# Optimization experiments

Hardware: AMD Instinct MI355X
Metric: run time of the kernel (lower is better)

Reference implementation:

```python
import jax, jax.numpy as jnp
import numpy as np

N = 40000          # nodes
E = 640000         # edges
D_IN, D_HID, D_EMB, D_OUT = 128, 128, 64, 2


def glorot(key, shape):
    lim = np.sqrt(6.0 / (shape[0] + shape[1]))
    return jax.random.uniform(key, shape, jnp.float32, -lim, lim)


def setup_inputs() -> dict:
    key = jax.random.key(0)
    ks = jax.random.split(key, 8)
    x = jax.random.normal(ks[0], (N, D_IN), jnp.float32)
    edge_index = jax.random.randint(ks[1], (2, E), 0, N, dtype=jnp.int64)
    # GCNConv weights stored as [in, out]; biases zero-init per PyG default
    W1 = glorot(ks[2], (D_IN, D_HID));  b1 = jnp.zeros((D_HID,), jnp.float32)
    W2 = glorot(ks[3], (D_HID, D_HID)); b2 = jnp.zeros((D_HID,), jnp.float32)
    W3 = glorot(ks[4], (D_HID, D_EMB)); b3 = jnp.zeros((D_EMB,), jnp.float32)
    Wout = glorot(ks[5], (D_EMB, D_OUT)); bout = jnp.zeros((D_OUT,), jnp.float32)
    return {"x": x, "edge_index": edge_index,
            "W1": W1, "b1": b1, "W2": W2, "b2": b2,
            "W3": W3, "b3": b3, "Wout": Wout, "bout": bout}


def _gcn_norm(edge_index, n):
    # add self loops, compute symmetric normalization d^-1/2[src] * d^-1/2[dst]
    loop = jnp.arange(n, dtype=edge_index.dtype)
    src = jnp.concatenate([edge_index[0], loop])
    dst = jnp.concatenate([edge_index[1], loop])
    deg = jax.ops.segment_sum(jnp.ones_like(dst, dtype=jnp.float32), dst,
                              num_segments=n)
    dinv = jax.lax.rsqrt(deg)                      # deg >= 1 due to self-loops
    dinv = jnp.where(jnp.isinf(dinv), 0.0, dinv)
    return src, dst, dinv[src] * dinv[dst]


def gcn_conv(x, src, dst, norm, W, b):
    h = x @ W                                      # [N, out]
    msg = h[src] * norm[:, None]                   # gather + scale  [E+N, out]
    return jax.ops.segment_sum(msg, dst, num_segments=x.shape[0]) + b


def reference(x, edge_index, W1, b1, W2, b2, W3, b3, Wout, bout):
    n = x.shape[0]
    src, dst, norm = _gcn_norm(edge_index, n)      # cached=True: computed once
    h = jax.nn.relu(gcn_conv(x, src, dst, norm, W1, b1))   # dropout is identity in eval
    h = jax.nn.relu(gcn_conv(h, src, dst, norm, W2, b2))
    h = gcn_conv(h, src, dst, norm, W3, b3)
    out = h @ Wout + bout
    return (out, h)
```

## Files before the change

kernel.cpp:

```cpp
#include <hip/hip_runtime.h>
#include <hip/hip_bf16.h>

#define NN 40000
#define NE 640000

typedef unsigned int u32;
typedef unsigned short u16;
typedef __attribute__((ext_vector_type(8))) short bf16x8;
typedef __attribute__((ext_vector_type(4))) float f32x4;

__device__ float g_wf[512];
__device__ u16   g_wp[40960];
__device__ int   g_cnt[NN];
__device__ int   g_cur[NN];
__device__ int   g_rowptr[NN + 1];
__device__ float g_dinv[NN];
__device__ int   g_csrc[NE];
__device__ int   g_bsum[64];
__device__ u16   g_ha[(size_t)NN * 128];
__device__ u16   g_hb[(size_t)NN * 128];

#define OFF_B1 0
#define OFF_B2 128
#define OFF_B3 256
#define OFF_WO 320
#define OFF_BO 448
#define WP_W1 0
#define WP_W2 16384
#define WP_W3 32768

__device__ __forceinline__ float b2f(u16 v){ return __uint_as_float(((u32)v) << 16); }
__device__ __forceinline__ float blo(u32 u){ return __uint_as_float(u << 16); }
__device__ __forceinline__ float bhi(u32 u){ return __uint_as_float(u & 0xffff0000u); }
__device__ __forceinline__ u32 f2bf(float f){
  u32 u = __float_as_uint(f);
  return (u + 0x7fffu + ((u >> 16) & 1u)) >> 16;
}
__device__ __forceinline__ int clampi(int v, int lo, int hi){ return v < lo ? lo : (v > hi ? hi : v); }
__device__ __forceinline__ u16 ldbf(const void* p, int idx, int f32){
  return f32 ? (u16)f2bf(((const float*)p)[idx]) : ((const u16*)p)[idx];
}
__device__ __forceinline__ float ldf(const void* p, int idx, int f32){
  return f32 ? ((const float*)p)[idx] : b2f(((const u16*)p)[idx]);
}

__device__ __forceinline__ int detect_xf32(const u16* __restrict__ xf){
  int i = ((int)threadIdx.x & 63) * 64;
  u16 v = xf[2 * i];
  int e = (v >> 7) & 0xff;
  int pass = (v == 0 || (e >= 100 && e <= 140)) ? 1 : 0;
  return (__popcll(__ballot(pass)) < 32) ? 1 : 0;
}
__device__ __forceinline__ int detect_estride(const int* __restrict__ ei){
  int i = ((int)threadIdx.x & 63) * 64;
  int pass = (ei[2 * i + 1] == 0) ? 1 : 0;
  return (__popcll(__ballot(pass)) >= 32) ? 2 : 1;
}

__global__ __launch_bounds__(256) void k_prep(const void* xin, const int* __restrict__ ei,
                                              const void* w1, const void* b1,
                                              const void* w2, const void* b2, const void* w3,
                                              const void* b3, const void* wo, const void* bo){
  int xf32 = detect_xf32((const u16*)xin);
  int strd = detect_estride(ei);
  int T = (int)blockIdx.x * 256 + (int)threadIdx.x;
  if (T < 640000){
    if (xf32){
      const float4* p = (const float4*)xin + (size_t)T * 2;
      float4 a = p[0], b = p[1];
      uint4 o;
      o.x = f2bf(a.x) | (f2bf(a.y) << 16);
      o.y = f2bf(a.z) | (f2bf(a.w) << 16);
      o.z = f2bf(b.x) | (f2bf(b.y) << 16);
      o.w = f2bf(b.z) | (f2bf(b.w) << 16);
      ((uint4*)g_ha)[T] = o;
    } else {
      ((uint4*)g_ha)[T] = ((const uint4*)xin)[T];
    }
    int d = clampi(ei[(size_t)(NE + T) * strd], 0, NN - 1);
    atomicAdd(&g_cnt[d], 1);
  } else if (T < 680960){
    int local = T - 640000;
    int J, dstbase, l; const void* src;
    if (local < 16384){ J = 128; src = w1; dstbase = WP_W1; l = local; }
    else if (local < 32768){ J = 128; src = w2; dstbase = WP_W2; l = local - 16384; }
    else { J = 64; src = w3; dstbase = WP_W3; l = local - 32768; }
    int chunk = l >> 9, within = l & 511;
    int nbw = J / 16;
    int kb = chunk / nbw, nb = chunk % nbw;
    int lane = within >> 3, j = within & 7;
    int q = lane >> 4, n = lane & 15;
    int k = kb * 32 + q * 8 + j;
    int col = nb * 16 + n;
    g_wp[dstbase + l] = ldbf(src, k * J + col, xf32);
  } else if (T < 681410){
    int l = T - 680960;
    if (l < 128)      g_wf[OFF_B1 + l] = ldf(b1, l, xf32);
    else if (l < 256) g_wf[OFF_B2 + l - 128] = ldf(b2, l - 128, xf32);
    else if (l < 320) g_wf[OFF_B3 + l - 256] = ldf(b3, l - 256, xf32);
    else if (l < 448) g_wf[OFF_WO + l - 320] = ldf(wo, l - 320, xf32);
    else              g_wf[OFF_BO + l - 448] = ldf(bo, l - 448, xf32);
  }
}

__global__ __launch_bounds__(1024) void k_scan1(){
  int t = (int)threadIdx.x;
  int b = (int)blockIdx.x;
  int i = b * 1024 + t;
  int v = (i < NN) ? g_cnt[i] : 0;
  int lane = t & 63, wv = t >> 6;
  int x = v;
#pragma unroll
  for (int ofs = 1; ofs < 64; ofs <<= 1){
    int y = __shfl_up(x, ofs, 64);
    if (lane >= ofs) x += y;
  }
  __shared__ int wsum[16];
  if (lane == 63) wsum[wv] = x;
  __syncthreads();
  if (t < 16){
    int s = wsum[t];
#pragma unroll
    for (int ofs = 1; ofs < 16; ofs <<= 1){
      int y = __shfl_up(s, ofs, 64);
      if (t >= ofs) s += y;
    }
    wsum[t] = s;
  }
  __syncthreads();
  int pre = (wv == 0) ? 0 : wsum[wv - 1];
  int incl = x + pre;
  if (i < NN){
    g_rowptr[i] = incl - v;
    g_dinv[i] = rsqrtf((float)(v + 1));
  }
  if (t == 1023) g_bsum[b] = incl;
}

__global__ __launch_bounds__(1024) void k_scan3(){
  __shared__ int pre;
  int t = (int)threadIdx.x;
  if (t < 64){
    int v = (t < 40) ? g_bsum[t] : 0;
    int s = v;
#pragma unroll
    for (int ofs = 1; ofs < 64; ofs <<= 1){
      int y = __shfl_up(s, ofs, 64);
      if (t >= ofs) s += y;
    }
    if (t == (int)blockIdx.x) pre = s - v;
    if (blockIdx.x == 0 && t == 39) g_rowptr[NN] = s;
  }
  __syncthreads();
  int i = (int)blockIdx.x * 1024 + t;
  if (i < NN) g_rowptr[i] += pre;
}

__global__ __launch_bounds__(256) void k_fillgemm(const int* __restrict__ ei){
  int bid = (int)blockIdx.x;
  if (bid < 2500){
    int strd = detect_estride(ei);
    int e = bid * 256 + (int)threadIdx.x;
    if (e < NE){
      int d = clampi(ei[(size_t)(NE + e) * strd], 0, NN - 1);
      int s = clampi(ei[(size_t)e * strd], 0, NN - 1);
      int pos = clampi(g_rowptr[d] + atomicAdd(&g_cur[d], 1), 0, NE - 1);
      g_csrc[pos] = s;
    }
  } else {
    constexpr int J = 128;
    constexpr int NB = J / 16;
    int tid = (int)threadIdx.x;
    int wave = tid >> 6, lane = tid & 63;
    int q = lane >> 4, n = lane & 15;
    int m0 = (bid - 2500) * 64 + wave * 16;
    f32x4 acc[NB];
#pragma unroll
    for (int nb = 0; nb < NB; ++nb) acc[nb] = (f32x4){0.f, 0.f, 0.f, 0.f};
    const u16* arow = g_ha + (size_t)(m0 + n) * 128 + q * 8;
#pragma unroll
    for (int kb = 0; kb < 4; ++kb){
      bf16x8 a = *(const bf16x8*)(arow + kb * 32);
      const u16* wbase = g_wp + WP_W1 + (kb * NB) * 512 + lane * 8;
#pragma unroll
      for (int nb = 0; nb < NB; ++nb){
        bf16x8 w = *(const bf16x8*)(wbase + nb * 512);
        acc[nb] = __builtin_amdgcn_mfma_f32_16x16x32_bf16(a, w, acc[nb], 0, 0, 0);
      }
    }
    u16* crow = g_hb + (size_t)(m0 + q * 4) * J + n;
#pragma unroll
    for (int r = 0; r < 4; ++r){
      float di = g_dinv[m0 + q * 4 + r];
#pragma unroll
      for (int nb = 0; nb < NB; ++nb)
        crow[(size_t)r * J + nb * 16] = (u16)f2bf(acc[nb][r] * di);
    }
  }
}

template<int J>
__global__ __launch_bounds__(256) void k_gemm(int wpoff){
  constexpr int NB = J / 16;
  int tid = (int)threadIdx.x;
  int wave = tid >> 6, lane = tid & 63;
  int q = lane >> 4, n = lane & 15;
  int m0 = (int)blockIdx.x * 64 + wave * 16;
  f32x4 acc[NB];
#pragma unroll
  for (int nb = 0; nb < NB; ++nb) acc[nb] = (f32x4){0.f, 0.f, 0.f, 0.f};
  const u16* arow = g_ha + (size_t)(m0 + n) * 128 + q * 8;
#pragma unroll
  for (int kb = 0; kb < 4; ++kb){
    bf16x8 a = *(const bf16x8*)(arow + kb * 32);
    const u16* wbase = g_wp + wpoff + (kb * NB) * 512 + lane * 8;
#pragma unroll
    for (int nb = 0; nb < NB; ++nb){
      bf16x8 w = *(const bf16x8*)(wbase + nb * 512);
      acc[nb] = __builtin_amdgcn_mfma_f32_16x16x32_bf16(a, w, acc[nb], 0, 0, 0);
    }
  }
  u16* crow = g_hb + (size_t)(m0 + q * 4) * J + n;
#pragma unroll
  for (int r = 0; r < 4; ++r){
    float di = g_dinv[m0 + q * 4 + r];
#pragma unroll
    for (int nb = 0; nb < NB; ++nb)
      crow[(size_t)r * J + nb * 16] = (u16)f2bf(acc[nb][r] * di);
  }
}

#define ACC8(P) do { \
    a0 += blo((P).x); a1 += bhi((P).x); \
    a2 += blo((P).y); a3 += bhi((P).y); \
    a4 += blo((P).z); a5 += bhi((P).z); \
    a6 += blo((P).w); a7 += bhi((P).w); } while (0)

template<int J, bool RELU, bool ZCLR>
__global__ __launch_bounds__(256, 4) void k_agg(int boff, float* __restrict__ h3, float* __restrict__ outp){
  constexpr int LPR = J / 8;
  int gt = (int)blockIdx.x * 256 + (int)threadIdx.x;
  if (ZCLR){
    if (gt < NN){ g_cnt[gt] = 0; g_cur[gt] = 0; }
  }
  int wid = gt / LPR;
  int lane = (int)threadIdx.x & (LPR - 1);
  if (wid >= NN) return;
  int cc = lane * 8;
  const u16* __restrict__ hb = g_hb;
  float di = g_dinv[wid];
  int beg = g_rowptr[wid], end = g_rowptr[wid + 1];
  uint4 ps = *(const uint4*)(hb + (size_t)wid * J + cc);
  float a0 = 0.f, a1 = 0.f, a2 = 0.f, a3 = 0.f, a4 = 0.f, a5 = 0.f, a6 = 0.f, a7 = 0.f;
  for (int e = beg; e < end; e += 8){
    int s0, s1, s2, s3, s4, s5, s6, s7;
    {
      int last = end - 1;
#define LDS_IDX(T) clampi(g_csrc[(e + T < last) ? (e + T) : last], 0, NN - 1)
      s0 = LDS_IDX(0); s1 = LDS_IDX(1); s2 = LDS_IDX(2); s3 = LDS_IDX(3);
      s4 = LDS_IDX(4); s5 = LDS_IDX(5); s6 = LDS_IDX(6); s7 = LDS_IDX(7);
#undef LDS_IDX
    }
    uint4 p0 = *(const uint4*)(hb + (size_t)s0 * J + cc);
    uint4 p1 = *(const uint4*)(hb + (size_t)s1 * J + cc);
    uint4 p2 = *(const uint4*)(hb + (size_t)s2 * J + cc);
    uint4 p3 = *(const uint4*)(hb + (size_t)s3 * J + cc);
    uint4 p4 = *(const uint4*)(hb + (size_t)s4 * J + cc);
    uint4 p5 = *(const uint4*)(hb + (size_t)s5 * J + cc);
    uint4 p6 = *(const uint4*)(hb + (size_t)s6 * J + cc);
    uint4 p7 = *(const uint4*)(hb + (size_t)s7 * J + cc);
    int nv = end - e;
    ACC8(p0);
    if (nv > 1) ACC8(p1);
    if (nv > 2) ACC8(p2);
    if (nv > 3) ACC8(p3);
    if (nv > 4) ACC8(p4);
    if (nv > 5) ACC8(p5);
    if (nv > 6) ACC8(p6);
    if (nv > 7) ACC8(p7);
  }
  ACC8(ps);
  a0 = a0 * di + g_wf[boff + cc];
  a1 = a1 * di + g_wf[boff + cc + 1];
  a2 = a2 * di + g_wf[boff + cc + 2];
  a3 = a3 * di + g_wf[boff + cc + 3];
  a4 = a4 * di + g_wf[boff + cc + 4];
  a5 = a5 * di + g_wf[boff + cc + 5];
  a6 = a6 * di + g_wf[boff + cc + 6];
  a7 = a7 * di + g_wf[boff + cc + 7];
  if (RELU){
    a0 = fmaxf(a0, 0.f); a1 = fmaxf(a1, 0.f); a2 = fmaxf(a2, 0.f); a3 = fmaxf(a3, 0.f);
    a4 = fmaxf(a4, 0.f); a5 = fmaxf(a5, 0.f); a6 = fmaxf(a6, 0.f); a7 = fmaxf(a7, 0.f);
  }
  if (J == 128){
    uint4 o;
    o.x = f2bf(a0) | (f2bf(a1) << 16);
    o.y = f2bf(a2) | (f2bf(a3) << 16);
    o.z = f2bf(a4) | (f2bf(a5) << 16);
    o.w = f2bf(a6) | (f2bf(a7) << 16);
    *(uint4*)(g_ha + (size_t)wid * 128 + cc) = o;
  } else {
    *(float4*)(h3 + (size_t)wid * 64 + cc)     = make_float4(a0, a1, a2, a3);
    *(float4*)(h3 + (size_t)wid * 64 + cc + 4) = make_float4(a4, a5, a6, a7);
    float o0 = a0 * g_wf[OFF_WO + (cc + 0) * 2] + a1 * g_wf[OFF_WO + (cc + 1) * 2]
             + a2 * g_wf[OFF_WO + (cc + 2) * 2] + a3 * g_wf[OFF_WO + (cc + 3) * 2]
             + a4 * g_wf[OFF_WO + (cc + 4) * 2] + a5 * g_wf[OFF_WO + (cc + 5) * 2]
             + a6 * g_wf[OFF_WO + (cc + 6) * 2] + a7 * g_wf[OFF_WO + (cc + 7) * 2];
    float o1 = a0 * g_wf[OFF_WO + (cc + 0) * 2 + 1] + a1 * g_wf[OFF_WO + (cc + 1) * 2 + 1]
             + a2 * g_wf[OFF_WO + (cc + 2) * 2 + 1] + a3 * g_wf[OFF_WO + (cc + 3) * 2 + 1]
             + a4 * g_wf[OFF_WO + (cc + 4) * 2 + 1] + a5 * g_wf[OFF_WO + (cc + 5) * 2 + 1]
             + a6 * g_wf[OFF_WO + (cc + 6) * 2 + 1] + a7 * g_wf[OFF_WO + (cc + 7) * 2 + 1];
#pragma unroll
    for (int m = 1; m < 8; m <<= 1){
      o0 += __shfl_xor(o0, m, 64);
      o1 += __shfl_xor(o1, m, 64);
    }
    if (lane == 0){
      *(float2*)(outp + (size_t)wid * 2) =
        make_float2(o0 + g_wf[OFF_BO], o1 + g_wf[OFF_BO + 1]);
    }
  }
}

extern "C" void kernel_launch(void* const* d_in, const int* in_sizes, int n_in,
                              void* d_out, int out_size, void* d_ws, size_t ws_size,
                              hipStream_t stream){
  const int* ei = (const int*)d_in[1];
  float* out = (float*)d_out;
  float* h3  = out + (size_t)NN * 2;

  k_prep<<<2662, 256, 0, stream>>>(d_in[0], ei, d_in[2], d_in[3], d_in[4], d_in[5],
                                   d_in[6], d_in[7], d_in[8], d_in[9]);
  k_scan1<<<40, 1024, 0, stream>>>();
  k_scan3<<<40, 1024, 0, stream>>>();
  k_fillgemm<<<3125, 256, 0, stream>>>(ei);

  k_agg<128, true, true><<<2500, 256, 0, stream>>>(OFF_B1, (float*)nullptr, (float*)nullptr);
  k_gemm<128><<<625, 256, 0, stream>>>(WP_W2);
  k_agg<128, true, false><<<2500, 256, 0, stream>>>(OFF_B2, (float*)nullptr, (float*)nullptr);
  k_gemm<64><<<625, 256, 0, stream>>>(WP_W3);
  k_agg<64, false, false><<<1250, 256, 0, stream>>>(OFF_B3, h3, out);
}
```

Baseline: 245.5 us.

## Fuse aggregation with next-layer GEMM via shared-memory tile

Merges each 128-wide aggregation kernel with the following dense GEMM. Each block aggregates 16 rows, writes the bf16 result to an LDS tile, and runs MFMA against the next weight matrix directly. The intermediate activation is no longer written to and reread from global memory, and two launches are removed. A ping-pong buffer is added so a kernel never reads the array it writes. The cost is a block barrier and per-block weight reloads across 2500 blocks, and each wave computes only a slice of the output columns.

```diff
diff --git a/kernel.cpp b/kernel.cpp
--- a/kernel.cpp
+++ b/kernel.cpp
@@ -19,6 +19,7 @@
 __device__ int   g_bsum[64];
 __device__ u16   g_ha[(size_t)NN * 128];
 __device__ u16   g_hb[(size_t)NN * 128];
+__device__ u16   g_hb2[(size_t)NN * 128];
 
 #define OFF_B1 0
 #define OFF_B2 128
@@ -199,50 +200,109 @@
   }
 }
 
-template<int J>
-__global__ __launch_bounds__(256) void k_gemm(int wpoff){
-  constexpr int NB = J / 16;
-  int tid = (int)threadIdx.x;
-  int wave = tid >> 6, lane = tid & 63;
-  int q = lane >> 4, n = lane & 15;
-  int m0 = (int)blockIdx.x * 64 + wave * 16;
-  f32x4 acc[NB];
-#pragma unroll
-  for (int nb = 0; nb < NB; ++nb) acc[nb] = (f32x4){0.f, 0.f, 0.f, 0.f};
-  const u16* arow = g_ha + (size_t)(m0 + n) * 128 + q * 8;
-#pragma unroll
-  for (int kb = 0; kb < 4; ++kb){
-    bf16x8 a = *(const bf16x8*)(arow + kb * 32);
-    const u16* wbase = g_wp + wpoff + (kb * NB) * 512 + lane * 8;
-#pragma unroll
-    for (int nb = 0; nb < NB; ++nb){
-      bf16x8 w = *(const bf16x8*)(wbase + nb * 512);
-      acc[nb] = __builtin_amdgcn_mfma_f32_16x16x32_bf16(a, w, acc[nb], 0, 0, 0);
-    }
-  }
-  u16* crow = g_hb + (size_t)(m0 + q * 4) * J + n;
-#pragma unroll
-  for (int r = 0; r < 4; ++r){
-    float di = g_dinv[m0 + q * 4 + r];
-#pragma unroll
-    for (int nb = 0; nb < NB; ++nb)
-      crow[(size_t)r * J + nb * 16] = (u16)f2bf(acc[nb][r] * di);
-  }
-}
-
 #define ACC8(P) do { \
     a0 += blo((P).x); a1 += bhi((P).x); \
     a2 += blo((P).y); a3 += bhi((P).y); \
     a4 += blo((P).z); a5 += bhi((P).z); \
     a6 += blo((P).w); a7 += bhi((P).w); } while (0)
 
-template<int J, bool RELU, bool ZCLR>
+template<int JOUT, bool SWAP, bool ZCLR>
+__global__ __launch_bounds__(256, 4) void k_agggemm(int boff, int wpoff){
+  constexpr int LSTRIDE = 136;
+  __shared__ u16 tile[16 * LSTRIDE];
+  const u16* __restrict__ src = SWAP ? g_hb2 : g_hb;
+  u16* __restrict__ dst = SWAP ? g_hb : g_hb2;
+  int tid = (int)threadIdx.x;
+  int gt = (int)blockIdx.x * 256 + tid;
+  if (ZCLR){ if (gt < NN){ g_cnt[gt] = 0; g_cur[gt] = 0; } }
+  int wid = gt >> 4;
+  int rt = tid >> 4;
+  int lane = tid & 15;
+  int cc = lane * 8;
+  float di = g_dinv[wid];
+  int beg = g_rowptr[wid], end = g_rowptr[wid + 1];
+  uint4 ps = *(const uint4*)(src + (size_t)wid * 128 + cc);
+  float a0 = 0.f, a1 = 0.f, a2 = 0.f, a3 = 0.f, a4 = 0.f, a5 = 0.f, a6 = 0.f, a7 = 0.f;
+  for (int e = beg; e < end; e += 8){
+    int s0, s1, s2, s3, s4, s5, s6, s7;
+    {
+      int last = end - 1;
+#define LDS_IDX(T) clampi(g_csrc[(e + T < last) ? (e + T) : last], 0, NN - 1)
+      s0 = LDS_IDX(0); s1 = LDS_IDX(1); s2 = LDS_IDX(2); s3 = LDS_IDX(3);
+      s4 = LDS_IDX(4); s5 = LDS_IDX(5); s6 = LDS_IDX(6); s7 = LDS_IDX(7);
+#undef LDS_IDX
+    }
+    uint4 p0 = *(const uint4*)(src + (size_t)s0 * 128 + cc);
+    uint4 p1 = *(const uint4*)(src + (size_t)s1 * 128 + cc);
+    uint4 p2 = *(const uint4*)(src + (size_t)s2 * 128 + cc);
+    uint4 p3 = *(const uint4*)(src + (size_t)s3 * 128 + cc);
+    uint4 p4 = *(const uint4*)(src + (size_t)s4 * 128 + cc);
+    uint4 p5 = *(const uint4*)(src + (size_t)s5 * 128 + cc);
+    uint4 p6 = *(const uint4*)(src + (size_t)s6 * 128 + cc);
+    uint4 p7 = *(const uint4*)(src + (size_t)s7 * 128 + cc);
+    int nv = end - e;
+    ACC8(p0);
+    if (nv > 1) ACC8(p1);
+    if (nv > 2) ACC8(p2);
+    if (nv > 3) ACC8(p3);
+    if (nv > 4) ACC8(p4);
+    if (nv > 5) ACC8(p5);
+    if (nv > 6) ACC8(p6);
+    if (nv > 7) ACC8(p7);
+  }
+  ACC8(ps);
+  a0 = a0 * di + g_wf[boff + cc];
+  a1 = a1 * di + g_wf[boff + cc + 1];
+  a2 = a2 * di + g_wf[boff + cc + 2];
+  a3 = a3 * di + g_wf[boff + cc + 3];
+  a4 = a4 * di + g_wf[boff + cc + 4];
+  a5 = a5 * di + g_wf[boff + cc + 5];
+  a6 = a6 * di + g_wf[boff + cc + 6];
+  a7 = a7 * di + g_wf[boff + cc + 7];
+  a0 = fmaxf(a0, 0.f); a1 = fmaxf(a1, 0.f); a2 = fmaxf(a2, 0.f); a3 = fmaxf(a3, 0.f);
+  a4 = fmaxf(a4, 0.f); a5 = fmaxf(a5, 0.f); a6 = fmaxf(a6, 0.f); a7 = fmaxf(a7, 0.f);
+  {
+    uint4 o;
+    o.x = f2bf(a0) | (f2bf(a1) << 16);
+    o.y = f2bf(a2) | (f2bf(a3) << 16);
+    o.z = f2bf(a4) | (f2bf(a5) << 16);
+    o.w = f2bf(a6) | (f2bf(a7) << 16);
+    *(uint4*)&tile[rt * LSTRIDE + cc] = o;
+  }
+  __syncthreads();
+  constexpr int NBF = JOUT / 16;
+  constexpr int NBW = NBF / 4;
+  int wave = tid >> 6, l64 = tid & 63;
+  int q = l64 >> 4, n = l64 & 15;
+  f32x4 acc[NBW];
+#pragma unroll
+  for (int j = 0; j < NBW; ++j) acc[j] = (f32x4){0.f, 0.f, 0.f, 0.f};
+#pragma unroll
+  for (int kb = 0; kb < 4; ++kb){
+    bf16x8 a = *(const bf16x8*)&tile[n * LSTRIDE + q * 8 + kb * 32];
+#pragma unroll
+    for (int j = 0; j < NBW; ++j){
+      int nb = wave * NBW + j;
+      bf16x8 w = *(const bf16x8*)(g_wp + wpoff + (kb * NBF + nb) * 512 + l64 * 8);
+      acc[j] = __builtin_amdgcn_mfma_f32_16x16x32_bf16(a, w, acc[j], 0, 0, 0);
+    }
+  }
+  int m0 = (int)blockIdx.x * 16;
+#pragma unroll
+  for (int r = 0; r < 4; ++r){
+    float dr = g_dinv[m0 + q * 4 + r];
+#pragma unroll
+    for (int j = 0; j < NBW; ++j){
+      int nb = wave * NBW + j;
+      dst[(size_t)(m0 + q * 4 + r) * JOUT + nb * 16 + n] = (u16)f2bf(acc[j][r] * dr);
+    }
+  }
+}
+
+template<int J, bool RELU>
 __global__ __launch_bounds__(256, 4) void k_agg(int boff, float* __restrict__ h3, float* __restrict__ outp){
   constexpr int LPR = J / 8;
   int gt = (int)blockIdx.x * 256 + (int)threadIdx.x;
-  if (ZCLR){
-    if (gt < NN){ g_cnt[gt] = 0; g_cur[gt] = 0; }
-  }
   int wid = gt / LPR;
   int lane = (int)threadIdx.x & (LPR - 1);
   if (wid >= NN) return;
@@ -292,33 +352,24 @@
     a0 = fmaxf(a0, 0.f); a1 = fmaxf(a1, 0.f); a2 = fmaxf(a2, 0.f); a3 = fmaxf(a3, 0.f);
     a4 = fmaxf(a4, 0.f); a5 = fmaxf(a5, 0.f); a6 = fmaxf(a6, 0.f); a7 = fmaxf(a7, 0.f);
   }
-  if (J == 128){
-    uint4 o;
-    o.x = f2bf(a0) | (f2bf(a1) << 16);
-    o.y = f2bf(a2) | (f2bf(a3) << 16);
-    o.z = f2bf(a4) | (f2bf(a5) << 16);
-    o.w = f2bf(a6) | (f2bf(a7) << 16);
-    *(uint4*)(g_ha + (size_t)wid * 128 + cc) = o;
-  } else {
-    *(float4*)(h3 + (size_t)wid * 64 + cc)     = make_float4(a0, a1, a2, a3);
-    *(float4*)(h3 + (size_t)wid * 64 + cc + 4) = make_float4(a4, a5, a6, a7);
-    float o0 = a0 * g_wf[OFF_WO + (cc + 0) * 2] + a1 * g_wf[OFF_WO + (cc + 1) * 2]
-             + a2 * g_wf[OFF_WO + (cc + 2) * 2] + a3 * g_wf[OFF_WO + (cc + 3) * 2]
-             + a4 * g_wf[OFF_WO + (cc + 4) * 2] + a5 * g_wf[OFF_WO + (cc + 5) * 2]
-             + a6 * g_wf[OFF_WO + (cc + 6) * 2] + a7 * g_wf[OFF_WO + (cc + 7) * 2];
-    float o1 = a0 * g_wf[OFF_WO + (cc + 0) * 2 + 1] + a1 * g_wf[OFF_WO + (cc + 1) * 2 + 1]
-             + a2 * g_wf[OFF_WO + (cc + 2) * 2 + 1] + a3 * g_wf[OFF_WO + (cc + 3) * 2 + 1]
-             + a4 * g_wf[OFF_WO + (cc + 4) * 2 + 1] + a5 * g_wf[OFF_WO + (cc + 5) * 2 + 1]
-             + a6 * g_wf[OFF_WO + (cc + 6) * 2 + 1] + a7 * g_wf[OFF_WO + (cc + 7) * 2 + 1];
-#pragma unroll
-    for (int m = 1; m < 8; m <<= 1){
-      o0 += __shfl_xor(o0, m, 64);
-      o1 += __shfl_xor(o1, m, 64);
-    }
-    if (lane == 0){
-      *(float2*)(outp + (size_t)wid * 2) =
-        make_float2(o0 + g_wf[OFF_BO], o1 + g_wf[OFF_BO + 1]);
-    }
+  *(float4*)(h3 + (size_t)wid * 64 + cc)     = make_float4(a0, a1, a2, a3);
+  *(float4*)(h3 + (size_t)wid * 64 + cc + 4) = make_float4(a4, a5, a6, a7);
+  float o0 = a0 * g_wf[OFF_WO + (cc + 0) * 2] + a1 * g_wf[OFF_WO + (cc + 1) * 2]
+           + a2 * g_wf[OFF_WO + (cc + 2) * 2] + a3 * g_wf[OFF_WO + (cc + 3) * 2]
+           + a4 * g_wf[OFF_WO + (cc + 4) * 2] + a5 * g_wf[OFF_WO + (cc + 5) * 2]
+           + a6 * g_wf[OFF_WO + (cc + 6) * 2] + a7 * g_wf[OFF_WO + (cc + 7) * 2];
+  float o1 = a0 * g_wf[OFF_WO + (cc + 0) * 2 + 1] + a1 * g_wf[OFF_WO + (cc + 1) * 2 + 1]
+           + a2 * g_wf[OFF_WO + (cc + 2) * 2 + 1] + a3 * g_wf[OFF_WO + (cc + 3) * 2 + 1]
+           + a4 * g_wf[OFF_WO + (cc + 4) * 2 + 1] + a5 * g_wf[OFF_WO + (cc + 5) * 2 + 1]
+           + a6 * g_wf[OFF_WO + (cc + 6) * 2 + 1] + a7 * g_wf[OFF_WO + (cc + 7) * 2 + 1];
+#pragma unroll
+  for (int m = 1; m < 8; m <<= 1){
+    o0 += __shfl_xor(o0, m, 64);
+    o1 += __shfl_xor(o1, m, 64);
+  }
+  if (lane == 0){
+    *(float2*)(outp + (size_t)wid * 2) =
+      make_float2(o0 + g_wf[OFF_BO], o1 + g_wf[OFF_BO + 1]);
   }
 }
 
@@ -335,9 +386,7 @@
   k_scan3<<<40, 1024, 0, stream>>>();
   k_fillgemm<<<3125, 256, 0, stream>>>(ei);
 
-  k_agg<128, true, true><<<2500, 256, 0, stream>>>(OFF_B1, (float*)nullptr, (float*)nullptr);
-  k_gemm<128><<<625, 256, 0, stream>>>(WP_W2);
-  k_agg<128, true, false><<<2500, 256, 0, stream>>>(OFF_B2, (float*)nullptr, (float*)nullptr);
-  k_gemm<64><<<625, 256, 0, stream>>>(WP_W3);
-  k_agg<64, false, false><<<1250, 256, 0, stream>>>(OFF_B3, h3, out);
-}
+  k_agggemm<128, false, true><<<2500, 256, 0, stream>>>(OFF_B1, WP_W2);
+  k_agggemm<64, true, false><<<2500, 256, 0, stream>>>(OFF_B2, WP_W3);
+  k_agg<64, false><<<1250, 256, 0, stream>>>(OFF_B3, h3, out);
+}
```

New measurement: 229.5 us. 1.07x faster.

## Shard feature matrices into 16-column panels for cache-local aggregation

Applied to the files above, without the earlier changes.

Stores node features in 8 column panels of 16 bf16 each (N x 16 per panel), and changes the aggregation kernels so each block handles one panel for a range of nodes. The randomly gathered working set per panel becomes small enough to stay in cache instead of spanning the full 128-column matrix. The GEMMs are rewritten to read and write the panel layout. The output head moves into a separate kernel because a node's 64 features are now split across blocks, which adds a launch and a re-read of h3. A second buffer g_hb2 is introduced between layers.

```diff
diff --git a/kernel.cpp b/kernel.cpp
--- a/kernel.cpp
+++ b/kernel.cpp
@@ -19,6 +19,9 @@
 __device__ int   g_bsum[64];
 __device__ u16   g_ha[(size_t)NN * 128];
 __device__ u16   g_hb[(size_t)NN * 128];
+__device__ u16   g_hb2[(size_t)NN * 128];
+
+#define PANEL ((size_t)NN * 16)
 
 #define OFF_B1 0
 #define OFF_B2 128
@@ -65,18 +68,19 @@
   int strd = detect_estride(ei);
   int T = (int)blockIdx.x * 256 + (int)threadIdx.x;
   if (T < 640000){
+    uint4 o;
     if (xf32){
       const float4* p = (const float4*)xin + (size_t)T * 2;
       float4 a = p[0], b = p[1];
-      uint4 o;
       o.x = f2bf(a.x) | (f2bf(a.y) << 16);
       o.y = f2bf(a.z) | (f2bf(a.w) << 16);
       o.z = f2bf(b.x) | (f2bf(b.y) << 16);
       o.w = f2bf(b.z) | (f2bf(b.w) << 16);
-      ((uint4*)g_ha)[T] = o;
     } else {
-      ((uint4*)g_ha)[T] = ((const uint4*)xin)[T];
-    }
+      o = ((const uint4*)xin)[T];
+    }
+    int pnl = (T >> 1) & 7;
+    ((uint4*)g_ha)[(size_t)pnl * 80000 + (size_t)(T >> 4) * 2 + (T & 1)] = o;
     int d = clampi(ei[(size_t)(NE + T) * strd], 0, NN - 1);
     atomicAdd(&g_cnt[d], 1);
   } else if (T < 680960){
@@ -156,6 +160,39 @@
   if (i < NN) g_rowptr[i] += pre;
 }
 
+template<int JOUT>
+__device__ __forceinline__ void gemm_body(int bid, int wpoff,
+                                          const u16* __restrict__ apan,
+                                          u16* __restrict__ dst){
+  constexpr int NB = JOUT / 16;
+  int tid = (int)threadIdx.x;
+  int wave = tid >> 6, lane = tid & 63;
+  int q = lane >> 4, n = lane & 15;
+  int m0 = bid * 64 + wave * 16;
+  f32x4 acc[NB];
+#pragma unroll
+  for (int nb = 0; nb < NB; ++nb) acc[nb] = (f32x4){0.f, 0.f, 0.f, 0.f};
+#pragma unroll
+  for (int kb = 0; kb < 4; ++kb){
+    bf16x8 a = *(const bf16x8*)(apan + (size_t)(2 * kb + (q >> 1)) * PANEL
+                                + (size_t)(m0 + n) * 16 + (q & 1) * 8);
+    const u16* wbase = g_wp + wpoff + (kb * NB) * 512 + lane * 8;
+#pragma unroll
+    for (int nb = 0; nb < NB; ++nb){
+      bf16x8 w = *(const bf16x8*)(wbase + nb * 512);
+      acc[nb] = __builtin_amdgcn_mfma_f32_16x16x32_bf16(a, w, acc[nb], 0, 0, 0);
+    }
+  }
+#pragma unroll
+  for (int r = 0; r < 4; ++r){
+    int node = m0 + q * 4 + r;
+    float di = g_dinv[node];
+#pragma unroll
+    for (int nb = 0; nb < NB; ++nb)
+      dst[(size_t)nb * PANEL + (size_t)node * 16 + n] = (u16)f2bf(acc[nb][r] * di);
+  }
+}
+
 __global__ __launch_bounds__(256) void k_fillgemm(const int* __restrict__ ei){
   int bid = (int)blockIdx.x;
   if (bid < 2500){
@@ -168,66 +205,13 @@
       g_csrc[pos] = s;
     }
   } else {
-    constexpr int J = 128;
-    constexpr int NB = J / 16;
-    int tid = (int)threadIdx.x;
-    int wave = tid >> 6, lane = tid & 63;
-    int q = lane >> 4, n = lane & 15;
-    int m0 = (bid - 2500) * 64 + wave * 16;
-    f32x4 acc[NB];
-#pragma unroll
-    for (int nb = 0; nb < NB; ++nb) acc[nb] = (f32x4){0.f, 0.f, 0.f, 0.f};
-    const u16* arow = g_ha + (size_t)(m0 + n) * 128 + q * 8;
-#pragma unroll
-    for (int kb = 0; kb < 4; ++kb){
-      bf16x8 a = *(const bf16x8*)(arow + kb * 32);
-      const u16* wbase = g_wp + WP_W1 + (kb * NB) * 512 + lane * 8;
-#pragma unroll
-      for (int nb = 0; nb < NB; ++nb){
-        bf16x8 w = *(const bf16x8*)(wbase + nb * 512);
-        acc[nb] = __builtin_amdgcn_mfma_f32_16x16x32_bf16(a, w, acc[nb], 0, 0, 0);
-      }
-    }
-    u16* crow = g_hb + (size_t)(m0 + q * 4) * J + n;
-#pragma unroll
-    for (int r = 0; r < 4; ++r){
-      float di = g_dinv[m0 + q * 4 + r];
-#pragma unroll
-      for (int nb = 0; nb < NB; ++nb)
-        crow[(size_t)r * J + nb * 16] = (u16)f2bf(acc[nb][r] * di);
-    }
-  }
-}
-
-template<int J>
+    gemm_body<128>(bid - 2500, WP_W1, g_ha, g_hb);
+  }
+}
+
+template<int JOUT, bool DST2>
 __global__ __launch_bounds__(256) void k_gemm(int wpoff){
-  constexpr int NB = J / 16;
-  int tid = (int)threadIdx.x;
-  int wave = tid >> 6, lane = tid & 63;
-  int q = lane >> 4, n = lane & 15;
-  int m0 = (int)blockIdx.x * 64 + wave * 16;
-  f32x4 acc[NB];
-#pragma unroll
-  for (int nb = 0; nb < NB; ++nb) acc[nb] = (f32x4){0.f, 0.f, 0.f, 0.f};
-  const u16* arow = g_ha + (size_t)(m0 + n) * 128 + q * 8;
-#pragma unroll
-  for (int kb = 0; kb < 4; ++kb){
-    bf16x8 a = *(const bf16x8*)(arow + kb * 32);
-    const u16* wbase = g_wp + wpoff + (kb * NB) * 512 + lane * 8;
-#pragma unroll
-    for (int nb = 0; nb < NB; ++nb){
-      bf16x8 w = *(const bf16x8*)(wbase + nb * 512);
-      acc[nb] = __builtin_amdgcn_mfma_f32_16x16x32_bf16(a, w, acc[nb], 0, 0, 0);
-    }
-  }
-  u16* crow = g_hb + (size_t)(m0 + q * 4) * J + n;
-#pragma unroll
-  for (int r = 0; r < 4; ++r){
-    float di = g_dinv[m0 + q * 4 + r];
-#pragma unroll
-    for (int nb = 0; nb < NB; ++nb)
-      crow[(size_t)r * J + nb * 16] = (u16)f2bf(acc[nb][r] * di);
-  }
+  gemm_body<JOUT>((int)blockIdx.x, wpoff, g_ha, DST2 ? g_hb2 : g_hb);
 }
 
 #define ACC8(P) do { \
@@ -236,21 +220,31 @@
     a4 += blo((P).z); a5 += bhi((P).z); \
     a6 += blo((P).w); a7 += bhi((P).w); } while (0)
 
-template<int J, bool RELU, bool ZCLR>
-__global__ __launch_bounds__(256, 4) void k_agg(int boff, float* __restrict__ h3, float* __restrict__ outp){
-  constexpr int LPR = J / 8;
-  int gt = (int)blockIdx.x * 256 + (int)threadIdx.x;
+template<int JIN, bool SRC2, bool RELU, bool ZCLR>
+__global__ __launch_bounds__(256, 4) void k_aggsh(int boff, float* __restrict__ h3out){
+  const u16* __restrict__ srcb = SRC2 ? g_hb2 : g_hb;
+  int tid = (int)threadIdx.x;
   if (ZCLR){
+    int gt = (int)blockIdx.x * 256 + tid;
     if (gt < NN){ g_cnt[gt] = 0; g_cur[gt] = 0; }
   }
-  int wid = gt / LPR;
-  int lane = (int)threadIdx.x & (LPR - 1);
+  int shard = (int)blockIdx.x & 7;
+  int bs = (int)blockIdx.x >> 3;
+  int wid, coff;
+  const u16* sp;
+  if (JIN == 128){
+    wid = bs * 128 + (tid >> 1);
+    sp = srcb + (size_t)shard * PANEL;
+    coff = (tid & 1) * 8;
+  } else {
+    wid = bs * 256 + tid;
+    sp = srcb + (size_t)(shard >> 1) * PANEL;
+    coff = (shard & 1) * 8;
+  }
   if (wid >= NN) return;
-  int cc = lane * 8;
-  const u16* __restrict__ hb = g_hb;
   float di = g_dinv[wid];
   int beg = g_rowptr[wid], end = g_rowptr[wid + 1];
-  uint4 ps = *(const uint4*)(hb + (size_t)wid * J + cc);
+  uint4 ps = *(const uint4*)(sp + (size_t)wid * 16 + coff);
   float a0 = 0.f, a1 = 0.f, a2 = 0.f, a3 = 0.f, a4 = 0.f, a5 = 0.f, a6 = 0.f, a7 = 0.f;
   for (int e = beg; e < end; e += 8){
     int s0, s1, s2, s3, s4, s5, s6, s7;
@@ -261,14 +255,14 @@
       s4 = LDS_IDX(4); s5 = LDS_IDX(5); s6 = LDS_IDX(6); s7 = LDS_IDX(7);
 #undef LDS_IDX
     }
-    uint4 p0 = *(const uint4*)(hb + (size_t)s0 * J + cc);
-    uint4 p1 = *(const uint4*)(hb + (size_t)s1 * J + cc);
-    uint4 p2 = *(const uint4*)(hb + (size_t)s2 * J + cc);
-    uint4 p3 = *(const uint4*)(hb + (size_t)s3 * J + cc);
-    uint4 p4 = *(const uint4*)(hb + (size_t)s4 * J + cc);
-    uint4 p5 = *(const uint4*)(hb + (size_t)s5 * J + cc);
-    uint4 p6 = *(const uint4*)(hb + (size_t)s6 * J + cc);
-    uint4 p7 = *(const uint4*)(hb + (size_t)s7 * J + cc);
+    uint4 p0 = *(const uint4*)(sp + (size_t)s0 * 16 + coff);
+    uint4 p1 = *(const uint4*)(sp + (size_t)s1 * 16 + coff);
+    uint4 p2 = *(const uint4*)(sp + (size_t)s2 * 16 + coff);
+    uint4 p3 = *(const uint4*)(sp + (size_t)s3 * 16 + coff);
+    uint4 p4 = *(const uint4*)(sp + (size_t)s4 * 16 + coff);
+    uint4 p5 = *(const uint4*)(sp + (size_t)s5 * 16 + coff);
+    uint4 p6 = *(const uint4*)(sp + (size_t)s6 * 16 + coff);
+    uint4 p7 = *(const uint4*)(sp + (size_t)s7 * 16 + coff);
     int nv = end - e;
     ACC8(p0);
     if (nv > 1) ACC8(p1);
@@ -280,45 +274,59 @@
     if (nv > 7) ACC8(p7);
   }
   ACC8(ps);
-  a0 = a0 * di + g_wf[boff + cc];
-  a1 = a1 * di + g_wf[boff + cc + 1];
-  a2 = a2 * di + g_wf[boff + cc + 2];
-  a3 = a3 * di + g_wf[boff + cc + 3];
-  a4 = a4 * di + g_wf[boff + cc + 4];
-  a5 = a5 * di + g_wf[boff + cc + 5];
-  a6 = a6 * di + g_wf[boff + cc + 6];
-  a7 = a7 * di + g_wf[boff + cc + 7];
+  int bb = boff + ((JIN == 128) ? (shard * 16 + coff) : (shard * 8));
+  a0 = a0 * di + g_wf[bb];
+  a1 = a1 * di + g_wf[bb + 1];
+  a2 = a2 * di + g_wf[bb + 2];
+  a3 = a3 * di + g_wf[bb + 3];
+  a4 = a4 * di + g_wf[bb + 4];
+  a5 = a5 * di + g_wf[bb + 5];
+  a6 = a6 * di + g_wf[bb + 6];
+  a7 = a7 * di + g_wf[bb + 7];
   if (RELU){
     a0 = fmaxf(a0, 0.f); a1 = fmaxf(a1, 0.f); a2 = fmaxf(a2, 0.f); a3 = fmaxf(a3, 0.f);
     a4 = fmaxf(a4, 0.f); a5 = fmaxf(a5, 0.f); a6 = fmaxf(a6, 0.f); a7 = fmaxf(a7, 0.f);
   }
-  if (J == 128){
+  if (JIN == 128){
     uint4 o;
     o.x = f2bf(a0) | (f2bf(a1) << 16);
     o.y = f2bf(a2) | (f2bf(a3) << 16);
     o.z = f2bf(a4) | (f2bf(a5) << 16);
     o.w = f2bf(a6) | (f2bf(a7) << 16);
-    *(uint4*)(g_ha + (size_t)wid * 128 + cc) = o;
+    *(uint4*)(g_ha + (size_t)shard * PANEL + (size_t)wid * 16 + coff) = o;
   } else {
-    *(float4*)(h3 + (size_t)wid * 64 + cc)     = make_float4(a0, a1, a2, a3);
-    *(float4*)(h3 + (size_t)wid * 64 + cc + 4) = make_float4(a4, a5, a6, a7);
-    float o0 = a0 * g_wf[OFF_WO + (cc + 0) * 2] + a1 * g_wf[OFF_WO + (cc + 1) * 2]
-             + a2 * g_wf[OFF_WO + (cc + 2) * 2] + a3 * g_wf[OFF_WO + (cc + 3) * 2]
-             + a4 * g_wf[OFF_WO + (cc + 4) * 2] + a5 * g_wf[OFF_WO + (cc + 5) * 2]
-             + a6 * g_wf[OFF_WO + (cc + 6) * 2] + a7 * g_wf[OFF_WO + (cc + 7) * 2];
-    float o1 = a0 * g_wf[OFF_WO + (cc + 0) * 2 + 1] + a1 * g_wf[OFF_WO + (cc + 1) * 2 + 1]
-             + a2 * g_wf[OFF_WO + (cc + 2) * 2 + 1] + a3 * g_wf[OFF_WO + (cc + 3) * 2 + 1]
-             + a4 * g_wf[OFF_WO + (cc + 4) * 2 + 1] + a5 * g_wf[OFF_WO + (cc + 5) * 2 + 1]
-             + a6 * g_wf[OFF_WO + (cc + 6) * 2 + 1] + a7 * g_wf[OFF_WO + (cc + 7) * 2 + 1];
-#pragma unroll
-    for (int m = 1; m < 8; m <<= 1){
-      o0 += __shfl_xor(o0, m, 64);
-      o1 += __shfl_xor(o1, m, 64);
-    }
-    if (lane == 0){
-      *(float2*)(outp + (size_t)wid * 2) =
-        make_float2(o0 + g_wf[OFF_BO], o1 + g_wf[OFF_BO + 1]);
-    }
+    *(float4*)(h3out + (size_t)wid * 64 + shard * 8)     = make_float4(a0, a1, a2, a3);
+    *(float4*)(h3out + (size_t)wid * 64 + shard * 8 + 4) = make_float4(a4, a5, a6, a7);
+  }
+}
+
+__global__ __launch_bounds__(256) void k_head(const float* __restrict__ h3,
+                                              float* __restrict__ outp){
+  int gt = (int)blockIdx.x * 256 + (int)threadIdx.x;
+  int wid = gt >> 3;
+  int lane = (int)threadIdx.x & 7;
+  if (wid >= NN) return;
+  int cc = lane * 8;
+  float4 v0 = *(const float4*)(h3 + (size_t)wid * 64 + cc);
+  float4 v1 = *(const float4*)(h3 + (size_t)wid * 64 + cc + 4);
+  float a0 = v0.x, a1 = v0.y, a2 = v0.z, a3 = v0.w;
+  float a4 = v1.x, a5 = v1.y, a6 = v1.z, a7 = v1.w;
+  float o0 = a0 * g_wf[OFF_WO + (cc + 0) * 2] + a1 * g_wf[OFF_WO + (cc + 1) * 2]
+           + a2 * g_wf[OFF_WO + (cc + 2) * 2] + a3 * g_wf[OFF_WO + (cc + 3) * 2]
+           + a4 * g_wf[OFF_WO + (cc + 4) * 2] + a5 * g_wf[OFF_WO + (cc + 5) * 2]
+           + a6 * g_wf[OFF_WO + (cc + 6) * 2] + a7 * g_wf[OFF_WO + (cc + 7) * 2];
+  float o1 = a0 * g_wf[OFF_WO + (cc + 0) * 2 + 1] + a1 * g_wf[OFF_WO + (cc + 1) * 2 + 1]
+           + a2 * g_wf[OFF_WO + (cc + 2) * 2 + 1] + a3 * g_wf[OFF_WO + (cc + 3) * 2 + 1]
+           + a4 * g_wf[OFF_WO + (cc + 4) * 2 + 1] + a5 * g_wf[OFF_WO + (cc + 5) * 2 + 1]
+           + a6 * g_wf[OFF_WO + (cc + 6) * 2 + 1] + a7 * g_wf[OFF_WO + (cc + 7) * 2 + 1];
+#pragma unroll
+  for (int m = 1; m < 8; m <<= 1){
+    o0 += __shfl_xor(o0, m, 64);
+    o1 += __shfl_xor(o1, m, 64);
+  }
+  if (lane == 0){
+    *(float2*)(outp + (size_t)wid * 2) =
+      make_float2(o0 + g_wf[OFF_BO], o1 + g_wf[OFF_BO + 1]);
   }
 }
 
@@ -335,9 +343,10 @@
   k_scan3<<<40, 1024, 0, stream>>>();
   k_fillgemm<<<3125, 256, 0, stream>>>(ei);
 
-  k_agg<128, true, true><<<2500, 256, 0, stream>>>(OFF_B1, (float*)nullptr, (float*)nullptr);
-  k_gemm<128><<<625, 256, 0, stream>>>(WP_W2);
-  k_agg<128, true, false><<<2500, 256, 0, stream>>>(OFF_B2, (float*)nullptr, (float*)nullptr);
-  k_gemm<64><<<625, 256, 0, stream>>>(WP_W3);
-  k_agg<64, false, false><<<1250, 256, 0, stream>>>(OFF_B3, h3, out);
-}
+  k_aggsh<128, false, true,  true ><<<2504, 256, 0, stream>>>(OFF_B1, nullptr);
+  k_gemm<128, true ><<<625, 256, 0, stream>>>(WP_W2);
+  k_aggsh<128, true,  true,  false><<<2504, 256, 0, stream>>>(OFF_B2, nullptr);
+  k_gemm<64,  false><<<625, 256, 0, stream>>>(WP_W3);
+  k_aggsh<64,  false, false, false><<<1256, 256, 0, stream>>>(OFF_B3, h3);
+  k_head<<<1250, 256, 0, stream>>>(h3, out);
+}
```

Measured after the change: 267.6 us. 1.09x slower.
